# Optimization experiments

Measured on AMD Instinct MI355X. Metric: run time of the kernel, lower is better.

The kernel has to match this reference:

```python
import jax, jax.numpy as jnp
import numpy as np

B, N = 512, 4
OBS, OBSU, ID = 128, 64, 16
STATE = OBS + OBSU - ID  # 176
M1, M2, G1, A = 256, 256, 256, 16
E = 128  # hypernet_embed


def setup_inputs() -> dict:
    key = jax.random.key(0)
    ks = jax.random.split(key, 24)

    def W(k, shape):
        return jax.random.normal(k, shape, dtype=jnp.float32) * 0.05

    inp = {"input": jax.random.normal(ks[0], (B, N, OBS + OBSU), dtype=jnp.float32)}
    # layer1_hypernet: Linear(ID, 10*E)
    inp["l1_W"] = W(ks[1], (10 * E, ID)); inp["l1_b"] = W(ks[2], (10 * E,))
    # hyper_net{i}_w / hyper_net{i}_b : Linear(E, in*out) / Linear(E, out)
    inp["w1W"] = W(ks[3], (STATE * M1, E)); inp["w1b"] = W(ks[4], (STATE * M1,))
    inp["b1W"] = W(ks[5], (M1, E));        inp["b1b"] = W(ks[6], (M1,))
    inp["w2W"] = W(ks[7], (M1 * M2, E));   inp["w2b"] = W(ks[8], (M1 * M2,))
    inp["b2W"] = W(ks[9], (M2, E));        inp["b2b"] = W(ks[10], (M2,))
    inp["w3W"] = W(ks[11], (M2 * M2, E));  inp["w3b"] = W(ks[12], (M2 * M2,))
    inp["b3W"] = W(ks[13], (M2, E));       inp["b3b"] = W(ks[14], (M2,))
    inp["w4W"] = W(ks[15], (M2 * G1, E));  inp["w4b"] = W(ks[16], (M2 * G1,))
    inp["b4W"] = W(ks[17], (G1, E));       inp["b4b"] = W(ks[18], (G1,))
    inp["w5W"] = W(ks[19], (G1 * A, E));   inp["w5b"] = W(ks[20], (G1 * A,))
    inp["b5W"] = W(ks[21], (A, E));        inp["b5b"] = W(ks[22], (A,))
    return inp


def reference(input, l1_W, l1_b, w1W, w1b, b1W, b1b, w2W, w2b, b2W, b2b,
              w3W, w3b, b3W, b3b, w4W, w4b, b4W, b4b, w5W, w5b, b5W, b5b):
    b, n, d = input.shape
    BN = b * n
    ids = input[..., -ID:].reshape(BN, ID)
    x = input[..., :-ID].reshape(BN, d - ID)  # [BN, STATE]
    # layer1_hypernet: ReLU(Linear(ID -> 10E))
    h = jax.nn.relu(ids @ l1_W.T + l1_b)  # [BN, 10E]
    chunk = lambda i: h[:, i * E:(i + 1) * E]

    def layer(x, iw, ib, wW, wb, bW, bb, out_dim, act):
        # generate per-sample weight [BN, in, out] and bias [BN, out]
        Wm = (chunk(iw) @ wW.T + wb).reshape(BN, x.shape[-1], out_dim)
        bm = chunk(ib) @ bW.T + bb
        y = jnp.einsum('bs,bsm->bm', x, Wm) + bm  # batched GEMV
        return jax.nn.relu(y) if act else y

    out = layer(x,   0, 1, w1W, w1b, b1W, b1b, M1, True)
    out = layer(out, 2, 3, w2W, w2b, b2W, b2b, M2, True)
    out = layer(out, 4, 5, w3W, w3b, b3W, b3b, M2, True)
    out = layer(out, 6, 7, w4W, w4b, b4W, b4b, G1, False)  # no ReLU after layer 4
    out = layer(out, 8, 9, w5W, w5b, b5W, b5b, A, True)
    return out.reshape(b, n, A)
```

## Files before the change

### kernel.cpp

```cpp
#include <hip/hip_runtime.h>
#include <hip/hip_bf16.h>

#define E_ 128
#define NSAMP 2048

typedef __attribute__((ext_vector_type(8))) short short8;
typedef __attribute__((ext_vector_type(4))) float floatx4;

__device__ __forceinline__ ushort f2b(float f) {
    union { __hip_bfloat16 h; ushort u; } cv;
    cv.h = __float2bfloat16(f);
    return cv.u;
}

__device__ __forceinline__ void gload_lds16(const ushort* g, ushort* l) {
    __builtin_amdgcn_global_load_lds(
        (const __attribute__((address_space(1))) void*)g,
        (__attribute__((address_space(3))) void*)l, 16, 0, 0);
}

__global__ void hyper_h(const float* __restrict__ input, const float* __restrict__ l1W,
                        const float* __restrict__ l1b, float* __restrict__ h)
{
    int b = blockIdx.x / 5;
    int o = (blockIdx.x % 5) * 256 + threadIdx.x;
    const float* ids = input + (size_t)b * 192 + 176;
    const float* w = l1W + (size_t)o * 16;
    float a = l1b[o];
#pragma unroll
    for (int i = 0; i < 16; i += 4) {
        float4 wv = *(const float4*)(w + i);
        a += ids[i] * wv.x + ids[i + 1] * wv.y + ids[i + 2] * wv.z + ids[i + 3] * wv.w;
    }
    h[(size_t)b * 1280 + o] = fmaxf(a, 0.f);
}

__global__ void x0_t(const float* __restrict__ input, float* __restrict__ xT0)
{
    int idx = blockIdx.x * 256 + threadIdx.x;
    int s = idx >> 11, b = idx & 2047;
    xT0[idx] = input[(size_t)b * 192 + s];
}

__global__ void cvt_bf16(const float* __restrict__ src, ushort* __restrict__ dst, int n)
{
    int i = (blockIdx.x * 256 + threadIdx.x) * 8;
    if (i >= n) return;
    float4 a = *(const float4*)(src + i);
    float4 b = *(const float4*)(src + i + 4);
    union { ushort o[8]; uint4 v; } u;
    u.o[0] = f2b(a.x); u.o[1] = f2b(a.y); u.o[2] = f2b(a.z); u.o[3] = f2b(a.w);
    u.o[4] = f2b(b.x); u.o[5] = f2b(b.y); u.o[6] = f2b(b.z); u.o[7] = f2b(b.w);
    *(uint4*)(dst + i) = u.v;
}

__global__ void cvt_bias(const float* __restrict__ bW, const float* __restrict__ wb,
                         ushort* __restrict__ dst, int S, int M)
{
    int idx = blockIdx.x * 256 + threadIdx.x;
    int slice = idx / (M * E_);
    int rem = idx - slice * (M * E_);
    int m = rem / E_, e = rem - m * E_;
    ushort v;
    if (slice == 0) {
        v = f2b(bW[(size_t)m * E_ + e]);
    } else {
        int s = (slice - 1) * 128 + e;
        v = (s < S) ? f2b(wb[(size_t)s * M + m]) : (ushort)0;
    }
    dst[(size_t)(S + slice) * M * E_ + rem] = v;
}

__global__ __launch_bounds__(256, 2) void gemm_big(
    const ushort* __restrict__ wWb, const float* __restrict__ h,
    const float* __restrict__ xT, float* __restrict__ partial,
    int S, int iw, int ksplit, int btiles, int ntiles)
{
    __shared__ ushort As[128 * 64];
    __shared__ ushort Bs[128 * 64];

    const int tid = threadIdx.x;
    const int bt = blockIdx.x % btiles;
    const int nt = (blockIdx.x / btiles) % ntiles;
    const int ks = blockIdx.x / (btiles * ntiles);
    const int b0 = bt * 128;
    const int m0 = nt * 128;
    const int total_s = S + 3;
    const int base = total_s / ksplit;
    const int rem = total_s - base * ksplit;
    const int s0 = ks * base + min(ks, rem);
    const int s1 = s0 + base + (ks < rem ? 1 : 0);

    const int lane = tid & 63;
    const int wave = tid >> 6;
    const int quad = lane >> 4;
    const int lr = lane & 15;
    const int wm0 = (wave >> 1) * 64;
    const int wn0 = (wave & 1) * 64;

    const int tb = tid >> 3;
    const int teg = tid & 7;
    const int aswz = (teg ^ (tb & 7)) * 8;

    const int brow = lane >> 3;
    const int bgg = (lane & 7) ^ brow;

    float hreg[4][2][8];
#pragma unroll
    for (int k2 = 0; k2 < 4; ++k2) {
#pragma unroll
        for (int p = 0; p < 2; ++p) {
            const float* src = h + (size_t)(b0 + tb + 32 * k2) * 1280 + (size_t)iw * E_ + p * 64 + teg * 8;
            float4 v0 = *(const float4*)(src);
            float4 v1 = *(const float4*)(src + 4);
            hreg[k2][p][0] = v0.x; hreg[k2][p][1] = v0.y; hreg[k2][p][2] = v0.z; hreg[k2][p][3] = v0.w;
            hreg[k2][p][4] = v1.x; hreg[k2][p][5] = v1.y; hreg[k2][p][6] = v1.z; hreg[k2][p][7] = v1.w;
        }
    }

    floatx4 acc[4][4];
#pragma unroll
    for (int i = 0; i < 4; ++i)
#pragma unroll
        for (int j = 0; j < 4; ++j)
            acc[i][j] = (floatx4){0.f, 0.f, 0.f, 0.f};

    for (int s = s0; s < s1; ++s) {
        float xv[4];
        if (s < S) {
#pragma unroll
            for (int k2 = 0; k2 < 4; ++k2)
                xv[k2] = xT[(size_t)s * NSAMP + b0 + tb + 32 * k2];
        }

#pragma unroll
        for (int p = 0; p < 2; ++p) {
            __syncthreads();

#pragma unroll
            for (int t = 0; t < 4; ++t) {
                int rloc = wave * 32 + t * 8;
                const ushort* gp = wWb + ((size_t)s * 256 + m0 + rloc + brow) * E_ + p * 64 + bgg * 8;
                ushort* lp = &Bs[(size_t)rloc * 64] + lane * 8;
                gload_lds16(gp, lp);
            }

            if (s < S) {
#pragma unroll
                for (int k2 = 0; k2 < 4; ++k2) {
                    union { ushort o[8]; uint4 v; } u;
#pragma unroll
                    for (int j = 0; j < 8; ++j) u.o[j] = f2b(xv[k2] * hreg[k2][p][j]);
                    *(uint4*)&As[(size_t)(tb + 32 * k2) * 64 + aswz] = u.v;
                }
            } else if (s == S) {
#pragma unroll
                for (int k2 = 0; k2 < 4; ++k2) {
                    const float* src = h + (size_t)(b0 + tb + 32 * k2) * 1280
                                         + (size_t)(iw + 1) * E_ + p * 64 + teg * 8;
                    float4 v0 = *(const float4*)(src);
                    float4 v1 = *(const float4*)(src + 4);
                    union { ushort o[8]; uint4 v; } u;
                    u.o[0] = f2b(v0.x); u.o[1] = f2b(v0.y); u.o[2] = f2b(v0.z); u.o[3] = f2b(v0.w);
                    u.o[4] = f2b(v1.x); u.o[5] = f2b(v1.y); u.o[6] = f2b(v1.z); u.o[7] = f2b(v1.w);
                    *(uint4*)&As[(size_t)(tb + 32 * k2) * 64 + aswz] = u.v;
                }
            } else {
                int j0 = (s - S - 1) * 128 + p * 64 + teg * 8;
#pragma unroll
                for (int k2 = 0; k2 < 4; ++k2) {
                    int b = b0 + tb + 32 * k2;
                    union { ushort o[8]; uint4 v; } u;
#pragma unroll
                    for (int jj = 0; jj < 8; ++jj) {
                        int sp = j0 + jj;
                        u.o[jj] = (sp < S) ? f2b(xT[(size_t)sp * NSAMP + b]) : (ushort)0;
                    }
                    *(uint4*)&As[(size_t)(tb + 32 * k2) * 64 + aswz] = u.v;
                }
            }

            __syncthreads();

#pragma unroll
            for (int kk = 0; kk < 2; ++kk) {
                const int swz = ((kk * 4 + quad) ^ (lr & 7)) * 8;
                short8 af[4], bfr[4];
#pragma unroll
                for (int i = 0; i < 4; ++i)
                    af[i] = *(const short8*)&As[(size_t)(wm0 + i * 16 + lr) * 64 + swz];
#pragma unroll
                for (int j = 0; j < 4; ++j)
                    bfr[j] = *(const short8*)&Bs[(size_t)(wn0 + j * 16 + lr) * 64 + swz];
#pragma unroll
                for (int i = 0; i < 4; ++i)
#pragma unroll
                    for (int j = 0; j < 4; ++j)
                        acc[i][j] = __builtin_amdgcn_mfma_f32_16x16x32_bf16(af[i], bfr[j], acc[i][j], 0, 0, 0);
            }
        }
    }

    float* dst = partial + (size_t)ks * NSAMP * 256;
#pragma unroll
    for (int i = 0; i < 4; ++i)
#pragma unroll
        for (int j = 0; j < 4; ++j)
#pragma unroll
            for (int r = 0; r < 4; ++r) {
                int row = wm0 + i * 16 + quad * 4 + r;
                int col = wn0 + j * 16 + lr;
                dst[(size_t)(b0 + row) * 256 + m0 + col] = acc[i][j][r];
            }
}

template<int BM, int BN, int WROWS, int WCOLS>
__global__ __launch_bounds__(256, 2) void gemm_k(
    const ushort* __restrict__ wWb, const float* __restrict__ h,
    const float* __restrict__ xT, float* __restrict__ partial,
    int S, int M, int iw, int ksplit, int btiles, int ntiles)
{
    constexpr int SM = BM / WROWS / 16;
    constexpr int SN = BN / WCOLS / 16;
    constexpr int ASLOTS = BM * 8 / 256;
    constexpr int LDA = 72;

    __shared__ ushort As[BM][LDA];
    __shared__ ushort Bs[BN][LDA];

    const int tid = threadIdx.x;
    const int bt = blockIdx.x % btiles;
    const int nt = (blockIdx.x / btiles) % ntiles;
    const int ks = blockIdx.x / (btiles * ntiles);
    const int b0 = bt * BM;
    const int m0 = nt * BN;
    const int total_s = S + 3;
    const int base = total_s / ksplit;
    const int rem = total_s - base * ksplit;
    const int s0 = ks * base + min(ks, rem);
    const int s1 = s0 + base + (ks < rem ? 1 : 0);

    const int lane = tid & 63;
    const int wave = tid >> 6;
    const int quad = lane >> 4;
    const int lr = lane & 15;
    const int wm0 = (wave / WCOLS) * (BM / WROWS);
    const int wn0 = (wave % WCOLS) * (BN / WCOLS);

    const int tb = tid >> 3;
    const int teg = tid & 7;

    float hreg[ASLOTS][2][8];
#pragma unroll
    for (int k2 = 0; k2 < ASLOTS; ++k2) {
        int b = tb + 32 * k2;
#pragma unroll
        for (int p = 0; p < 2; ++p) {
            const float* src = h + (size_t)(b0 + b) * 1280 + (size_t)iw * E_ + p * 64 + teg * 8;
            float4 v0 = *(const float4*)(src);
            float4 v1 = *(const float4*)(src + 4);
            hreg[k2][p][0] = v0.x; hreg[k2][p][1] = v0.y; hreg[k2][p][2] = v0.z; hreg[k2][p][3] = v0.w;
            hreg[k2][p][4] = v1.x; hreg[k2][p][5] = v1.y; hreg[k2][p][6] = v1.z; hreg[k2][p][7] = v1.w;
        }
    }

    floatx4 acc[SM][SN];
#pragma unroll
    for (int i = 0; i < SM; ++i)
#pragma unroll
        for (int j = 0; j < SN; ++j)
            acc[i][j] = (floatx4){0.f, 0.f, 0.f, 0.f};

    for (int s = s0; s < s1; ++s) {
        float xv[ASLOTS];
        if (s < S) {
#pragma unroll
            for (int k2 = 0; k2 < ASLOTS; ++k2)
                xv[k2] = xT[(size_t)s * NSAMP + b0 + tb + 32 * k2];
        }

#pragma unroll
        for (int p = 0; p < 2; ++p) {
            if (s < S) {
#pragma unroll
                for (int k2 = 0; k2 < ASLOTS; ++k2) {
                    union { ushort o[8]; uint4 v; } u;
#pragma unroll
                    for (int j = 0; j < 8; ++j) u.o[j] = f2b(xv[k2] * hreg[k2][p][j]);
                    *(uint4*)&As[tb + 32 * k2][teg * 8] = u.v;
                }
            } else if (s == S) {
#pragma unroll
                for (int k2 = 0; k2 < ASLOTS; ++k2) {
                    const float* src = h + (size_t)(b0 + tb + 32 * k2) * 1280
                                         + (size_t)(iw + 1) * E_ + p * 64 + teg * 8;
                    float4 v0 = *(const float4*)(src);
                    float4 v1 = *(const float4*)(src + 4);
                    union { ushort o[8]; uint4 v; } u;
                    u.o[0] = f2b(v0.x); u.o[1] = f2b(v0.y); u.o[2] = f2b(v0.z); u.o[3] = f2b(v0.w);
                    u.o[4] = f2b(v1.x); u.o[5] = f2b(v1.y); u.o[6] = f2b(v1.z); u.o[7] = f2b(v1.w);
                    *(uint4*)&As[tb + 32 * k2][teg * 8] = u.v;
                }
            } else {
                int j0 = (s - S - 1) * 128 + p * 64 + teg * 8;
#pragma unroll
                for (int k2 = 0; k2 < ASLOTS; ++k2) {
                    int b = b0 + tb + 32 * k2;
                    union { ushort o[8]; uint4 v; } u;
#pragma unroll
                    for (int jj = 0; jj < 8; ++jj) {
                        int sp = j0 + jj;
                        u.o[jj] = (sp < S) ? f2b(xT[(size_t)sp * NSAMP + b]) : (ushort)0;
                    }
                    *(uint4*)&As[tb + 32 * k2][teg * 8] = u.v;
                }
            }
#pragma unroll
            for (int slot = tid; slot < BN * 8; slot += 256) {
                int m = slot >> 3, eg2 = slot & 7;
                *(uint4*)&Bs[m][eg2 * 8] =
                    *(const uint4*)(wWb + ((size_t)s * M + m0 + m) * E_ + p * 64 + eg2 * 8);
            }
            __syncthreads();
#pragma unroll
            for (int kk = 0; kk < 2; ++kk) {
                short8 af[SM], bfr[SN];
#pragma unroll
                for (int i = 0; i < SM; ++i)
                    af[i] = *(const short8*)&As[wm0 + i * 16 + lr][kk * 32 + quad * 8];
#pragma unroll
                for (int j = 0; j < SN; ++j)
                    bfr[j] = *(const short8*)&Bs[wn0 + j * 16 + lr][kk * 32 + quad * 8];
#pragma unroll
                for (int i = 0; i < SM; ++i)
#pragma unroll
                    for (int j = 0; j < SN; ++j)
                        acc[i][j] = __builtin_amdgcn_mfma_f32_16x16x32_bf16(af[i], bfr[j], acc[i][j], 0, 0, 0);
            }
            __syncthreads();
        }
    }

    float* dst = partial + (size_t)ks * NSAMP * M;
#pragma unroll
    for (int i = 0; i < SM; ++i)
#pragma unroll
        for (int j = 0; j < SN; ++j)
#pragma unroll
            for (int r = 0; r < 4; ++r) {
                int row = wm0 + i * 16 + quad * 4 + r;
                int col = wn0 + j * 16 + lr;
                dst[(size_t)(b0 + row) * M + m0 + col] = acc[i][j][r];
            }
}

__global__ void reduce_mid(const float* __restrict__ partial, const float* __restrict__ bb,
                           float* __restrict__ xTn, int KS, int relu)
{
    __shared__ float t[32][33];
    const int b0 = (blockIdx.x >> 3) * 32;
    const int m0 = (blockIdx.x & 7) * 32;
    const int mo = threadIdx.x & 31;
    const int bs0 = threadIdx.x >> 5;
    const float bv = bb[m0 + mo];
#pragma unroll
    for (int r = 0; r < 4; ++r) {
        const int bs = bs0 + 8 * r;
        const size_t off = (size_t)(b0 + bs) * 256 + m0 + mo;
        float a0 = 0.f, a1 = 0.f, a2 = 0.f, a3 = 0.f;
#pragma unroll
        for (int k = 0; k < 16; k += 4) {
            a0 += partial[(size_t)(k + 0) * (NSAMP * 256) + off];
            a1 += partial[(size_t)(k + 1) * (NSAMP * 256) + off];
            a2 += partial[(size_t)(k + 2) * (NSAMP * 256) + off];
            a3 += partial[(size_t)(k + 3) * (NSAMP * 256) + off];
        }
        float a = (a0 + a1) + (a2 + a3) + bv;
        if (relu) a = fmaxf(a, 0.f);
        t[bs][mo] = a;
    }
    __syncthreads();
    const int bo = threadIdx.x & 31;
    const int ms0 = threadIdx.x >> 5;
#pragma unroll
    for (int r = 0; r < 4; ++r) {
        const int ms = ms0 + 8 * r;
        xTn[(size_t)(m0 + ms) * NSAMP + b0 + bo] = t[bo][ms];
    }
}

__global__ void reduce_out(const float* __restrict__ partial, const float* __restrict__ bb,
                           float* __restrict__ out, int KS)
{
    int idx = blockIdx.x * 256 + threadIdx.x;
    float a0 = 0.f, a1 = 0.f, a2 = 0.f, a3 = 0.f;
#pragma unroll
    for (int k = 0; k < 32; k += 4) {
        a0 += partial[(size_t)(k + 0) * (NSAMP * 16) + idx];
        a1 += partial[(size_t)(k + 1) * (NSAMP * 16) + idx];
        a2 += partial[(size_t)(k + 2) * (NSAMP * 16) + idx];
        a3 += partial[(size_t)(k + 3) * (NSAMP * 16) + idx];
    }
    out[idx] = fmaxf((a0 + a1) + (a2 + a3) + bb[idx & 15], 0.f);
}

extern "C" void kernel_launch(void* const* d_in, const int* in_sizes, int n_in,
                              void* d_out, int out_size, void* d_ws, size_t ws_size,
                              hipStream_t stream)
{
    const float* input = (const float*)d_in[0];
    const float* l1W   = (const float*)d_in[1];
    const float* l1b   = (const float*)d_in[2];

    char* ws = (char*)d_ws;
    ushort* wWb = (ushort*)(ws + 0);
    float* h    = (float*)(ws + 16975872);
    float* xT0  = (float*)(ws + 27461632);
    float* xT1  = (float*)(ws + 29558784);
    float* part = (float*)(ws + 31655936);

    hipLaunchKernelGGL(hyper_h, dim3(2048 * 5), dim3(256), 0, stream, input, l1W, l1b, h);
    hipLaunchKernelGGL(x0_t, dim3(176 * 2048 / 256), dim3(256), 0, stream, input, xT0);

    const int S_[5] = {176, 256, 256, 256, 256};
    const int M_[5] = {256, 256, 256, 256, 16};
    float* xt[2] = {xT0, xT1};

    for (int i = 0; i < 5; ++i) {
        const float* wW = (const float*)d_in[3 + 4 * i];
        const float* wb = (const float*)d_in[4 + 4 * i];
        const float* bW = (const float*)d_in[5 + 4 * i];
        const float* bb = (const float*)d_in[6 + 4 * i];
        float* xin = xt[i & 1];
        int n = S_[i] * M_[i] * E_;
        hipLaunchKernelGGL(cvt_bf16, dim3(n / 2048), dim3(256), 0, stream, wW, wWb, n);
        hipLaunchKernelGGL(cvt_bias, dim3(3 * M_[i] * E_ / 256), dim3(256), 0, stream,
                           bW, wb, wWb, S_[i], M_[i]);

        if (M_[i] == 256) {
            const int btiles = 16, ntiles = 2, ksplit = 16;
            hipLaunchKernelGGL(gemm_big, dim3(btiles * ntiles * ksplit), dim3(256), 0, stream,
                               wWb, h, xin, part, S_[i], 2 * i, ksplit, btiles, ntiles);
            hipLaunchKernelGGL(reduce_mid, dim3(512), dim3(256), 0, stream,
                               part, bb, xt[(i + 1) & 1], ksplit, (i < 3) ? 1 : 0);
        } else {
            const int btiles = 8, ntiles = 1, ksplit = 32;
            hipLaunchKernelGGL((gemm_k<256, 16, 4, 1>), dim3(btiles * ntiles * ksplit), dim3(256), 0, stream,
                               wWb, h, xin, part, S_[i], 16, 2 * i, ksplit, btiles, ntiles);
            hipLaunchKernelGGL(reduce_out, dim3(128), dim3(256), 0, stream,
                               part, bb, (float*)d_out, ksplit);
        }
    }
}
```

Before: 578.4 us.

## Double-buffer weight tiles in gemm_big and prefetch x into LDS; raise layer-5 ksplit

Restructures gemm_big's main loop into a software pipeline. Each weight tile is DMA'd into a double-buffered LDS slot two steps ahead, and the next A tile is generated while the MFMAs for the current step run. The x values for the block's s-range are staged once into shared memory, and setprio is raised around the MFMA section. The bias/extra rows keep the old synchronous path. Separately, the final layer's split-K factor is doubled and reduce_out is updated to match. This raises LDS use per block, which may reduce occupancy, and adds more partial-sum traffic for layer 5.

```diff
diff --git a/kernel.cpp b/kernel.cpp
--- a/kernel.cpp
+++ b/kernel.cpp
@@ -76,8 +76,9 @@
     const float* __restrict__ xT, float* __restrict__ partial,
     int S, int iw, int ksplit, int btiles, int ntiles)
 {
-    __shared__ ushort As[128 * 64];
-    __shared__ ushort Bs[128 * 64];
+    __shared__ __align__(16) ushort As[128 * 64];
+    __shared__ __align__(16) ushort Bs[2][128 * 64];
+    __shared__ __align__(16) float xs[17 * 128];
 
     const int tid = threadIdx.x;
     const int bt = blockIdx.x % btiles;
@@ -89,7 +90,10 @@
     const int base = total_s / ksplit;
     const int rem = total_s - base * ksplit;
     const int s0 = ks * base + min(ks, rem);
-    const int s1 = s0 + base + (ks < rem ? 1 : 0);
+    const int s1v = s0 + base + (ks < rem ? 1 : 0);
+    const int sE = min(s1v, S);
+    const int ns = sE - s0;
+    const int T = 2 * ns;
 
     const int lane = tid & 63;
     const int wave = tid >> 6;
@@ -118,6 +122,11 @@
         }
     }
 
+    for (int idx = tid; idx < ns * 128; idx += 256) {
+        int j = idx >> 7, bb2 = idx & 127;
+        xs[idx] = xT[(size_t)(s0 + j) * NSAMP + b0 + bb2];
+    }
+
     floatx4 acc[4][4];
 #pragma unroll
     for (int i = 0; i < 4; ++i)
@@ -125,35 +134,80 @@
         for (int j = 0; j < 4; ++j)
             acc[i][j] = (floatx4){0.f, 0.f, 0.f, 0.f};
 
-    for (int s = s0; s < s1; ++s) {
+    auto dmaB = [&](int s, int p, ushort* buf) {
+#pragma unroll
+        for (int t4 = 0; t4 < 4; ++t4) {
+            int rloc = wave * 32 + t4 * 8;
+            const ushort* gp = wWb + ((size_t)s * 256 + m0 + rloc + brow) * E_ + p * 64 + bgg * 8;
+            gload_lds16(gp, buf + (size_t)rloc * 64 + lane * 8);
+        }
+    };
+    auto genA = [&](int s, int p) {
         float xv[4];
-        if (s < S) {
-#pragma unroll
-            for (int k2 = 0; k2 < 4; ++k2)
-                xv[k2] = xT[(size_t)s * NSAMP + b0 + tb + 32 * k2];
-        }
-
+#pragma unroll
+        for (int k2 = 0; k2 < 4; ++k2) xv[k2] = xs[(s - s0) * 128 + tb + 32 * k2];
+#pragma unroll
+        for (int k2 = 0; k2 < 4; ++k2) {
+            union { ushort o[8]; uint4 v; } u;
+#pragma unroll
+            for (int j = 0; j < 8; ++j) u.o[j] = f2b(xv[k2] * hreg[k2][p][j]);
+            *(uint4*)&As[(size_t)(tb + 32 * k2) * 64 + aswz] = u.v;
+        }
+    };
+
+    genA(s0, 0);
+    __syncthreads();
+    __builtin_amdgcn_sched_barrier(0);
+    dmaB(s0, 0, Bs[0]);
+    dmaB(s0, 1, Bs[1]);
+
+    for (int t = 0; t < T; ++t) {
+        const int cur = t & 1;
+        if (t + 1 < T) {
+            asm volatile("s_waitcnt vmcnt(4) lgkmcnt(0)" ::: "memory");
+        } else {
+            asm volatile("s_waitcnt vmcnt(0) lgkmcnt(0)" ::: "memory");
+        }
+        __builtin_amdgcn_sched_barrier(0);
+        __builtin_amdgcn_s_barrier();
+        __builtin_amdgcn_sched_barrier(0);
+
+        short8 af[2][4], bfr[2][4];
+#pragma unroll
+        for (int kk = 0; kk < 2; ++kk) {
+            const int swz = ((kk * 4 + quad) ^ (lr & 7)) * 8;
+#pragma unroll
+            for (int i = 0; i < 4; ++i)
+                af[kk][i] = *(const short8*)&As[(size_t)(wm0 + i * 16 + lr) * 64 + swz];
+#pragma unroll
+            for (int j = 0; j < 4; ++j)
+                bfr[kk][j] = *(const short8*)&Bs[cur][(size_t)(wn0 + j * 16 + lr) * 64 + swz];
+        }
+        asm volatile("s_waitcnt lgkmcnt(0)" ::: "memory");
+        __builtin_amdgcn_sched_barrier(0);
+        __builtin_amdgcn_s_barrier();
+        __builtin_amdgcn_sched_barrier(0);
+
+        if (t + 2 < T) dmaB(s0 + ((t + 2) >> 1), (t + 2) & 1, Bs[cur]);
+        if (t + 1 < T) genA(s0 + ((t + 1) >> 1), (t + 1) & 1);
+
+        __builtin_amdgcn_s_setprio(1);
+#pragma unroll
+        for (int kk = 0; kk < 2; ++kk)
+#pragma unroll
+            for (int i = 0; i < 4; ++i)
+#pragma unroll
+                for (int j = 0; j < 4; ++j)
+                    acc[i][j] = __builtin_amdgcn_mfma_f32_16x16x32_bf16(af[kk][i], bfr[kk][j], acc[i][j], 0, 0, 0);
+        __builtin_amdgcn_s_setprio(0);
+    }
+
+    for (int s = sE; s < s1v; ++s) {
 #pragma unroll
         for (int p = 0; p < 2; ++p) {
             __syncthreads();
-
-#pragma unroll
-            for (int t = 0; t < 4; ++t) {
-                int rloc = wave * 32 + t * 8;
-                const ushort* gp = wWb + ((size_t)s * 256 + m0 + rloc + brow) * E_ + p * 64 + bgg * 8;
-                ushort* lp = &Bs[(size_t)rloc * 64] + lane * 8;
-                gload_lds16(gp, lp);
-            }
-
-            if (s < S) {
-#pragma unroll
-                for (int k2 = 0; k2 < 4; ++k2) {
-                    union { ushort o[8]; uint4 v; } u;
-#pragma unroll
-                    for (int j = 0; j < 8; ++j) u.o[j] = f2b(xv[k2] * hreg[k2][p][j]);
-                    *(uint4*)&As[(size_t)(tb + 32 * k2) * 64 + aswz] = u.v;
-                }
-            } else if (s == S) {
+            dmaB(s, p, Bs[0]);
+            if (s == S) {
 #pragma unroll
                 for (int k2 = 0; k2 < 4; ++k2) {
                     const float* src = h + (size_t)(b0 + tb + 32 * k2) * 1280
@@ -179,24 +233,22 @@
                     *(uint4*)&As[(size_t)(tb + 32 * k2) * 64 + aswz] = u.v;
                 }
             }
-
             __syncthreads();
-
 #pragma unroll
             for (int kk = 0; kk < 2; ++kk) {
                 const int swz = ((kk * 4 + quad) ^ (lr & 7)) * 8;
-                short8 af[4], bfr[4];
+                short8 af2[4], bf2[4];
 #pragma unroll
                 for (int i = 0; i < 4; ++i)
-                    af[i] = *(const short8*)&As[(size_t)(wm0 + i * 16 + lr) * 64 + swz];
+                    af2[i] = *(const short8*)&As[(size_t)(wm0 + i * 16 + lr) * 64 + swz];
 #pragma unroll
                 for (int j = 0; j < 4; ++j)
-                    bfr[j] = *(const short8*)&Bs[(size_t)(wn0 + j * 16 + lr) * 64 + swz];
+                    bf2[j] = *(const short8*)&Bs[0][(size_t)(wn0 + j * 16 + lr) * 64 + swz];
 #pragma unroll
                 for (int i = 0; i < 4; ++i)
 #pragma unroll
                     for (int j = 0; j < 4; ++j)
-                        acc[i][j] = __builtin_amdgcn_mfma_f32_16x16x32_bf16(af[i], bfr[j], acc[i][j], 0, 0, 0);
+                        acc[i][j] = __builtin_amdgcn_mfma_f32_16x16x32_bf16(af2[i], bf2[j], acc[i][j], 0, 0, 0);
             }
         }
     }
@@ -395,7 +447,7 @@
     int idx = blockIdx.x * 256 + threadIdx.x;
     float a0 = 0.f, a1 = 0.f, a2 = 0.f, a3 = 0.f;
 #pragma unroll
-    for (int k = 0; k < 32; k += 4) {
+    for (int k = 0; k < 64; k += 4) {
         a0 += partial[(size_t)(k + 0) * (NSAMP * 16) + idx];
         a1 += partial[(size_t)(k + 1) * (NSAMP * 16) + idx];
         a2 += partial[(size_t)(k + 2) * (NSAMP * 16) + idx];
@@ -444,7 +496,7 @@
             hipLaunchKernelGGL(reduce_mid, dim3(512), dim3(256), 0, stream,
                                part, bb, xt[(i + 1) & 1], ksplit, (i < 3) ? 1 : 0);
         } else {
-            const int btiles = 8, ntiles = 1, ksplit = 32;
+            const int btiles = 8, ntiles = 1, ksplit = 64;
             hipLaunchKernelGGL((gemm_k<256, 16, 4, 1>), dim3(btiles * ntiles * ksplit), dim3(256), 0, stream,
                                wWb, h, xin, part, S_[i], 16, 2 * i, ksplit, btiles, ntiles);
             hipLaunchKernelGGL(reduce_out, dim3(128), dim3(256), 0, stream,
```

After: 724.9 us. +25.3%, slower.
